# Optimization experiments

Measured on AMD Instinct MI355X. Metric: run time of the kernel, lower is better.

The kernel has to match this reference:

```python
import jax, jax.numpy as jnp
import numpy as np

EPS = 1e-8


def cos_loss(a, b):
    # a, b: [n, c, h, w]; cosine distance over channel dim, mean over rest
    a_norm = jnp.sqrt((a * a).sum(1, keepdims=True))
    b_norm = jnp.sqrt((b * b).sum(1, keepdims=True))
    cossim = ((a / (a_norm + EPS)) * (b / (b_norm + EPS))).sum(1)
    return (1.0 - cossim).mean()


def nn_feat_replace(a, b):
    # a: [1, c, h, w], b: [1, c, h2, w2]
    n, c, h, w = a.shape
    a_flat = a.reshape(n, c, -1)                    # [1, c, hw]
    b_flat = b.reshape(n, c, -1)                    # [1, c, h2w2]
    # normalize along channel dim (matches argmin_cos_distance's two-eps scheme)
    b_n = b_flat / (jnp.sqrt((b_flat * b_flat).sum(1, keepdims=True) + EPS) + EPS)
    a_n = a_flat / (jnp.sqrt((a_flat * a_flat).sum(1, keepdims=True) + EPS) + EPS)
    # full cosine-distance matrix: [1, hw, h2w2]
    d_mat = 1.0 - jnp.einsum('bci,bcj->bij', a_n, b_n)
    z_best = jnp.argmin(d_mat, axis=2)              # [1, hw]
    feat = jnp.take(b_flat, z_best[0], axis=2)      # gather: [1, c, hw]
    return feat.reshape(n, c, h, w)


def setup_inputs() -> dict:
    key = jax.random.key(0)
    k1, k2 = jax.random.split(key)
    a = jax.random.normal(k1, (1, 768, 128, 128), dtype=jnp.float32)
    b = jax.random.normal(k2, (1, 768, 128, 128), dtype=jnp.float32)
    return {"a": a, "b": b}


def reference(a, b):
    target = nn_feat_replace(a, b)
    return cos_loss(a, target)
```

## Files before the change

kernel.cpp:

```cpp
#include <hip/hip_runtime.h>
#include <stdint.h>

#define HW 16384
#define CDIM 768
#define EPSF 1e-8f

typedef float f32x4  __attribute__((ext_vector_type(4)));
typedef float f32x16 __attribute__((ext_vector_type(16)));
typedef int   i32x8  __attribute__((ext_vector_type(8)));
typedef uint32_t u32x4 __attribute__((ext_vector_type(4)));

__device__ inline void async16(const void* g, void* l) {
    __builtin_amdgcn_global_load_lds(
        (const __attribute__((address_space(1))) uint32_t*)g,
        (__attribute__((address_space(3))) uint32_t*)l, 16, 0, 0);
}

__device__ inline uint32_t pk4_fp8(float v0, float v1, float v2, float v3) {
    uint32_t r = __builtin_amdgcn_cvt_pk_fp8_f32(v0, v1, 0, false);
    r = __builtin_amdgcn_cvt_pk_fp8_f32(v2, v3, r, true);
    return r;
}

__global__ void __launch_bounds__(256)
transpose_fp8_norm(const float* __restrict__ a, const float* __restrict__ b,
                   uint8_t* __restrict__ at8, uint8_t* __restrict__ bn8,
                   float* __restrict__ sumsq_a, float* __restrict__ sumsq_b,
                   float* __restrict__ invdb) {
    const int z = blockIdx.z;
    const float* src = z ? b : a;
    uint8_t* dst = z ? bn8 : at8;
    float* sums = z ? sumsq_b : sumsq_a;
    const float mult = z ? 8.0f : 16.0f;

    __shared__ float tile[64][65];
    const int s0 = blockIdx.x * 64;
    const int tx = threadIdx.x & 63, ty = threadIdx.x >> 6;
    const int chgrp = tx & 15, rowsub = tx >> 4;
    uint32_t* dst32 = (uint32_t*)dst;

    float ss[4] = {0.0f, 0.0f, 0.0f, 0.0f};

#pragma unroll 1
    for (int cb = 0; cb < 12; ++cb) {
        const int c0 = cb * 64;
#pragma unroll
        for (int p = 0; p < 16; ++p) {
            int cl = p * 4 + ty;
            tile[cl][tx] = src[(size_t)(c0 + cl) * HW + s0 + tx];
        }
        __syncthreads();
#pragma unroll
        for (int p = 0; p < 4; ++p) {
            int sl = p * 16 + ty * 4 + rowsub;
            float v0 = tile[chgrp * 4 + 0][sl];
            float v1 = tile[chgrp * 4 + 1][sl];
            float v2 = tile[chgrp * 4 + 2][sl];
            float v3 = tile[chgrp * 4 + 3][sl];
            float part = v0 * v0 + v1 * v1 + v2 * v2 + v3 * v3;
            dst32[(size_t)(s0 + sl) * (CDIM / 4) + (c0 >> 2) + chgrp] =
                pk4_fp8(v0 * mult, v1 * mult, v2 * mult, v3 * mult);
#pragma unroll
            for (int m = 1; m < 16; m <<= 1) part += __shfl_xor(part, m, 64);
            ss[p] += part;
        }
        __syncthreads();
    }

#pragma unroll
    for (int p = 0; p < 4; ++p) {
        int sl = p * 16 + ty * 4 + rowsub;
        if (chgrp == 0) {
            float t = ss[p];
            sums[s0 + sl] = t;
            if (z) invdb[s0 + sl] = 1.0f / (sqrtf(t + EPSF) + EPSF);
        }
    }
}

__global__ void
gemm_argmax(const uint8_t* __restrict__ at8, const uint8_t* __restrict__ bn8,
            const float* __restrict__ invdb,
            unsigned long long* __restrict__ best) {
    __shared__ uint8_t Al[2 * 8192];
    __shared__ uint8_t Bl[2 * 8192];

    const int g = blockIdx.x;
    const int xcd    = g & 7;
    const int s      = g >> 3;
    const int super  = s >> 5;
    const int within = s & 31;
    const int si = super >> 4;
    const int sj = super & 15;
    const int it = xcd * 16 + si * 4 + (within & 3);
    const int jt = sj * 8 + (within >> 2);

    const int i0 = it * 128, j0 = jt * 128;
    const int tid = threadIdx.x;
    const int lane = tid & 63, w = tid >> 6;
    const int wi = w & 1, wj = w >> 1;
    const int l31 = lane & 31, hi = lane >> 5;

    f32x16 acc[2][2] = {};

    const int srow = lane >> 2;
    const int schunk = ((lane & 3) ^ ((lane >> 3) & 3)) * 16;
    const uint8_t* gA = at8 + (size_t)(i0 + w * 32 + srow) * CDIM + schunk;
    const uint8_t* gB = bn8 + (size_t)(j0 + w * 32 + srow) * CDIM + schunk;
    uint8_t* lA = Al + w * 2048;
    uint8_t* lB = Bl + w * 2048;

    const int rA0 = (wi * 64 + l31) * 64;
    const int rB0 = (wj * 64 + l31) * 64;
    const int c0 = ((hi * 2) ^ ((l31 >> 1) & 3)) * 16;

#define STAGE(bo, kk)                                         \
    do {                                                      \
        async16(gA + (kk),             lA + (bo));            \
        async16(gA + (kk) + 16 * CDIM, lA + (bo) + 1024);     \
        async16(gB + (kk),             lB + (bo));            \
        async16(gB + (kk) + 16 * CDIM, lB + (bo) + 1024);     \
    } while (0)

#define COMPUTE(bo)                                                          \
    do {                                                                     \
        i32x8 af0, af1, bg;                                                  \
        *(u32x4*)&af0       = *(const u32x4*)&Al[(bo) + rA0 + c0];           \
        *((u32x4*)&af0 + 1) = *(const u32x4*)&Al[(bo) + rA0 + (c0 ^ 16)];    \
        *(u32x4*)&af1       = *(const u32x4*)&Al[(bo) + rA0 + 2048 + c0];    \
        *((u32x4*)&af1 + 1) = *(const u32x4*)&Al[(bo) + rA0 + 2048 + (c0 ^ 16)]; \
        *(u32x4*)&bg        = *(const u32x4*)&Bl[(bo) + rB0 + c0];           \
        *((u32x4*)&bg + 1)  = *(const u32x4*)&Bl[(bo) + rB0 + (c0 ^ 16)];    \
        acc[0][0] = __builtin_amdgcn_mfma_scale_f32_32x32x64_f8f6f4(         \
            bg, af0, acc[0][0], 0, 0, 0, 0x7F7F7F7F, 0, 0x7F7F7F7F);         \
        acc[0][1] = __builtin_amdgcn_mfma_scale_f32_32x32x64_f8f6f4(         \
            bg, af1, acc[0][1], 0, 0, 0, 0x7F7F7F7F, 0, 0x7F7F7F7F);         \
        *(u32x4*)&bg        = *(const u32x4*)&Bl[(bo) + rB0 + 2048 + c0];    \
        *((u32x4*)&bg + 1)  = *(const u32x4*)&Bl[(bo) + rB0 + 2048 + (c0 ^ 16)]; \
        acc[1][0] = __builtin_amdgcn_mfma_scale_f32_32x32x64_f8f6f4(         \
            bg, af0, acc[1][0], 0, 0, 0, 0x7F7F7F7F, 0, 0x7F7F7F7F);         \
        acc[1][1] = __builtin_amdgcn_mfma_scale_f32_32x32x64_f8f6f4(         \
            bg, af1, acc[1][1], 0, 0, 0, 0x7F7F7F7F, 0, 0x7F7F7F7F);         \
    } while (0)

    STAGE(0, 0);
    asm volatile("s_waitcnt vmcnt(0)" ::: "memory");
    __builtin_amdgcn_s_barrier();

#pragma unroll 1
    for (int t = 0; t < 11; ++t) {
        const int bo = (t & 1) * 8192;
        STAGE(bo ^ 8192, (t + 1) * 64);
        COMPUTE(bo);
        asm volatile("s_waitcnt vmcnt(0)" ::: "memory");
        __builtin_amdgcn_s_barrier();
    }
    COMPUTE(8192);

#undef STAGE
#undef COMPUTE

    float bv[2] = {-1e30f, -1e30f};
    int   bj[2] = {0, 0};
#pragma unroll
    for (int nj = 0; nj < 2; ++nj) {
        const int jb = j0 + wj * 64 + nj * 32 + 4 * hi;
        f32x4 iv[4];
#pragma unroll
        for (int q = 0; q < 4; ++q)
            iv[q] = *(const f32x4*)&invdb[jb + 8 * q];
#pragma unroll
        for (int mi = 0; mi < 2; ++mi) {
#pragma unroll
            for (int r = 0; r < 16; ++r) {
                int j = jb + (r & 3) + 8 * (r >> 2);
                float v = acc[nj][mi][r] * iv[r >> 2][r & 3];
                if (v > bv[mi] || (v == bv[mi] && j < bj[mi])) {
                    bv[mi] = v; bj[mi] = j;
                }
            }
        }
    }
#pragma unroll
    for (int mi = 0; mi < 2; ++mi) {
        float ov = __shfl_xor(bv[mi], 32, 64);
        int   oj = __shfl_xor(bj[mi], 32, 64);
        if (ov > bv[mi] || (ov == bv[mi] && oj < bj[mi])) {
            bv[mi] = ov; bj[mi] = oj;
        }
        if (hi == 0) {
            int gi = i0 + wi * 64 + mi * 32 + l31;
            uint32_t u = __float_as_uint(bv[mi]);
            u = (u & 0x80000000u) ? ~u : (u | 0x80000000u);
            unsigned long long packed =
                ((unsigned long long)u << 32) | (uint32_t)(~(uint32_t)bj[mi]);
            atomicMax(&best[gi], packed);
        }
    }
}

__global__ void loss_reduce(const unsigned long long* __restrict__ best,
                            const float* __restrict__ sumsq_a,
                            const float* __restrict__ sumsq_b,
                            float* __restrict__ out) {
    int i = blockIdx.x * 256 + threadIdx.x;
    unsigned long long pk = best[i];
    uint32_t x = (uint32_t)(pk >> 32);
    float v = (x & 0x80000000u) ? __uint_as_float(x & 0x7fffffffu)
                                : __uint_as_float(~x);
    int j = (int)(~(uint32_t)pk);
    float sb = sumsq_b[j];
    float denb = sqrtf(sb + EPSF) + EPSF;
    float dot = v * denb * (1.0f / 128.0f);
    float cs = dot / ((sqrtf(sumsq_a[i]) + EPSF) * (sqrtf(sb) + EPSF));
    float term = 1.0f - cs;
#pragma unroll
    for (int m = 32; m; m >>= 1) term += __shfl_down(term, m, 64);
    __shared__ float red[4];
    int wv = threadIdx.x >> 6, lane = threadIdx.x & 63;
    if (lane == 0) red[wv] = term;
    __syncthreads();
    if (threadIdx.x == 0) {
        float ssum = (red[0] + red[1] + red[2] + red[3]) * (1.0f / HW);
        atomicAdd(out, ssum);
    }
}

extern "C" void kernel_launch(void* const* d_in, const int* in_sizes, int n_in,
                              void* d_out, int out_size, void* d_ws, size_t ws_size,
                              hipStream_t stream) {
    const float* a = (const float*)d_in[0];
    const float* b = (const float*)d_in[1];
    char* ws = (char*)d_ws;

    const size_t T_BYTES = (size_t)HW * CDIM;
    uint8_t* at8 = (uint8_t*)ws;
    uint8_t* bn8 = (uint8_t*)(ws + T_BYTES);
    float* sumsq_a = (float*)(ws + 2 * T_BYTES);
    float* sumsq_b = (float*)(ws + 2 * T_BYTES + HW * sizeof(float));
    unsigned long long* best =
        (unsigned long long*)(ws + 2 * T_BYTES + 2 * HW * sizeof(float));
    float* invdb = (float*)(ws + 2 * T_BYTES + 2 * HW * sizeof(float)
                            + HW * sizeof(unsigned long long));

    hipMemsetAsync(best, 0, HW * sizeof(unsigned long long), stream);
    hipMemsetAsync(d_out, 0, out_size * sizeof(float), stream);

    dim3 tg(HW / 64, 1, 2);
    transpose_fp8_norm<<<tg, 256, 0, stream>>>(a, b, at8, bn8,
                                               sumsq_a, sumsq_b, invdb);
    gemm_argmax<<<(HW / 128) * (HW / 128), 256, 0, stream>>>(at8, bn8, invdb, best);
    loss_reduce<<<HW / 256, 256, 0, stream>>>(best, sumsq_a, sumsq_b, (float*)d_out);
}
```

Measured before the change: 382.0 us.

## Restructure transpose kernel to stage fp8 output strips in LDS with vector stores

Each block of the transpose/quantize kernel now covers 32 spatial positions instead of 64 and loads input with 16-byte vector reads. It accumulates the whole 768-channel fp8 row for its strip in shared memory, then writes it to global memory in contiguous 16-byte chunks, replacing scattered 4-byte stores. The per-row sum of squares is kept in one accumulator and reduced once at the end rather than shuffled per tile. The trade-offs are more shared memory per block, shorter contiguous input reads per row, and twice as many blocks.

Result: no change. 382.7 us (+0.2%).

```diff
diff --git a/kernel.cpp b/kernel.cpp
--- a/kernel.cpp
+++ b/kernel.cpp
@@ -23,58 +23,67 @@
 }
 
 __global__ void __launch_bounds__(256)
-transpose_fp8_norm(const float* __restrict__ a, const float* __restrict__ b,
-                   uint8_t* __restrict__ at8, uint8_t* __restrict__ bn8,
-                   float* __restrict__ sumsq_a, float* __restrict__ sumsq_b,
-                   float* __restrict__ invdb) {
+transpose_fp8_strip(const float* __restrict__ a, const float* __restrict__ b,
+                    uint8_t* __restrict__ at8, uint8_t* __restrict__ bn8,
+                    float* __restrict__ sumsq_a, float* __restrict__ sumsq_b,
+                    float* __restrict__ invdb) {
     const int z = blockIdx.z;
     const float* src = z ? b : a;
     uint8_t* dst = z ? bn8 : at8;
     float* sums = z ? sumsq_b : sumsq_a;
     const float mult = z ? 8.0f : 16.0f;
 
-    __shared__ float tile[64][65];
-    const int s0 = blockIdx.x * 64;
-    const int tx = threadIdx.x & 63, ty = threadIdx.x >> 6;
-    const int chgrp = tx & 15, rowsub = tx >> 4;
-    uint32_t* dst32 = (uint32_t*)dst;
-
-    float ss[4] = {0.0f, 0.0f, 0.0f, 0.0f};
+    __shared__ float tile[64][33];
+    __shared__ uint32_t outT[32 * 192];
+
+    const int s0 = blockIdx.x * 32;
+    const int t = threadIdx.x;
+    const int l8 = t & 7;
+    const int sl = t >> 3;
+
+    float ss = 0.0f;
 
 #pragma unroll 1
     for (int cb = 0; cb < 12; ++cb) {
         const int c0 = cb * 64;
 #pragma unroll
-        for (int p = 0; p < 16; ++p) {
-            int cl = p * 4 + ty;
-            tile[cl][tx] = src[(size_t)(c0 + cl) * HW + s0 + tx];
+        for (int pass = 0; pass < 2; ++pass) {
+            int cl = pass * 32 + (t >> 3);
+            f32x4 v = *(const f32x4*)&src[(size_t)(c0 + cl) * HW + s0 + l8 * 4];
+            tile[cl][l8 * 4 + 0] = v[0];
+            tile[cl][l8 * 4 + 1] = v[1];
+            tile[cl][l8 * 4 + 2] = v[2];
+            tile[cl][l8 * 4 + 3] = v[3];
         }
         __syncthreads();
 #pragma unroll
-        for (int p = 0; p < 4; ++p) {
-            int sl = p * 16 + ty * 4 + rowsub;
+        for (int q = 0; q < 2; ++q) {
+            int chgrp = (t & 7) * 2 + q;
             float v0 = tile[chgrp * 4 + 0][sl];
             float v1 = tile[chgrp * 4 + 1][sl];
             float v2 = tile[chgrp * 4 + 2][sl];
             float v3 = tile[chgrp * 4 + 3][sl];
-            float part = v0 * v0 + v1 * v1 + v2 * v2 + v3 * v3;
-            dst32[(size_t)(s0 + sl) * (CDIM / 4) + (c0 >> 2) + chgrp] =
+            ss += v0 * v0 + v1 * v1 + v2 * v2 + v3 * v3;
+            outT[sl * 192 + cb * 16 + chgrp] =
                 pk4_fp8(v0 * mult, v1 * mult, v2 * mult, v3 * mult);
-#pragma unroll
-            for (int m = 1; m < 16; m <<= 1) part += __shfl_xor(part, m, 64);
-            ss[p] += part;
         }
         __syncthreads();
     }
 
 #pragma unroll
-    for (int p = 0; p < 4; ++p) {
-        int sl = p * 16 + ty * 4 + rowsub;
-        if (chgrp == 0) {
-            float t = ss[p];
-            sums[s0 + sl] = t;
-            if (z) invdb[s0 + sl] = 1.0f / (sqrtf(t + EPSF) + EPSF);
-        }
+    for (int m = 1; m < 8; m <<= 1) ss += __shfl_xor(ss, m, 64);
+    if ((t & 7) == 0) {
+        int s_idx = s0 + sl;
+        sums[s_idx] = ss;
+        if (z) invdb[s_idx] = 1.0f / (sqrtf(ss + EPSF) + EPSF);
+    }
+
+    uint8_t* gout = dst + (size_t)s0 * CDIM;
+    const uint8_t* lsrc = (const uint8_t*)outT;
+#pragma unroll
+    for (int p = 0; p < 6; ++p) {
+        int off = p * 4096 + t * 16;
+        *(u32x4*)(gout + off) = *(const u32x4*)(lsrc + off);
     }
 }
 
@@ -246,9 +255,9 @@
     hipMemsetAsync(best, 0, HW * sizeof(unsigned long long), stream);
     hipMemsetAsync(d_out, 0, out_size * sizeof(float), stream);
 
-    dim3 tg(HW / 64, 1, 2);
-    transpose_fp8_norm<<<tg, 256, 0, stream>>>(a, b, at8, bn8,
-                                               sumsq_a, sumsq_b, invdb);
+    dim3 tg(HW / 32, 1, 2);
+    transpose_fp8_strip<<<tg, 256, 0, stream>>>(a, b, at8, bn8,
+                                                sumsq_a, sumsq_b, invdb);
     gemm_argmax<<<(HW / 128) * (HW / 128), 256, 0, stream>>>(at8, bn8, invdb, best);
     loss_reduce<<<HW / 256, 256, 0, stream>>>(best, sumsq_a, sumsq_b, (float*)d_out);
 }
```
